# Performance work log

Measured on AMD Instinct MI355X. Metric: run time of the kernel, lower is better.

## Reference

```python
import jax, jax.numpy as jnp
import numpy as np

DIM = 4096
N_HEADS = 32
HEAD_DIM = 128
FFN = 11008
THETA = 10000.0
EPS = 1e-5
B, S, SP = 8, 1, 2048  # batch, decode seq_len, start_pos (valid cache length)


def rmsnorm(x, w):
    return x * jax.lax.rsqrt(jnp.mean(x * x, axis=-1, keepdims=True) + EPS) * w


def apply_rope(x, cos, sin):
    # x: [B, S, H, D]; interleaved-pair complex rotation as in Meta Llama
    xr = x[..., 0::2]
    xi = x[..., 1::2]
    out_r = xr * cos - xi * sin
    out_i = xr * sin + xi * cos
    return jnp.stack([out_r, out_i], axis=-1).reshape(x.shape)


def setup_inputs() -> dict:
    key = jax.random.key(0)
    ks = jax.random.split(key, 10)
    s = 0.02  # weight init scale
    return {
        "x": jax.random.normal(ks[0], (B, S, DIM), jnp.float32),
        "cache_k": jax.random.normal(ks[1], (B, SP, N_HEADS, HEAD_DIM), jnp.float32),
        "cache_v": jax.random.normal(ks[2], (B, SP, N_HEADS, HEAD_DIM), jnp.float32),
        "mask": jnp.zeros((B, N_HEADS, S, SP + S), jnp.float32),
        "wq": jax.random.normal(ks[3], (DIM, DIM), jnp.float32) * s,
        "wk": jax.random.normal(ks[4], (DIM, DIM), jnp.float32) * s,
        "wv": jax.random.normal(ks[5], (DIM, DIM), jnp.float32) * s,
        "wo": jax.random.normal(ks[6], (DIM, DIM), jnp.float32) * s,
        "w1": jax.random.normal(ks[7], (DIM, FFN), jnp.float32) * s,
        "w2": jax.random.normal(ks[8], (FFN, DIM), jnp.float32) * s,
        "w3": jax.random.normal(ks[9], (DIM, FFN), jnp.float32) * s,
        "attn_norm_w": jnp.ones((DIM,), jnp.float32),
        "ffn_norm_w": jnp.ones((DIM,), jnp.float32),
        "start_pos": SP,
    }


def reference(x, cache_k, cache_v, mask, wq, wk, wv, wo, w1, w2, w3, attn_norm_w, ffn_norm_w, start_pos):
    b, s, _ = x.shape
    # --- attention block ---
    h = rmsnorm(x, attn_norm_w)
    q = (h @ wq).reshape(b, s, N_HEADS, HEAD_DIM)
    k = (h @ wk).reshape(b, s, N_HEADS, HEAD_DIM)
    v = (h @ wv).reshape(b, s, N_HEADS, HEAD_DIM)
    # RoPE freqs for positions [start_pos, start_pos+s)
    inv_freq = 1.0 / (THETA ** (jnp.arange(0, HEAD_DIM, 2, dtype=jnp.float32) / HEAD_DIM))
    pos = (start_pos + jnp.arange(s)).astype(jnp.float32)
    ang = pos[:, None] * inv_freq[None, :]            # [s, HEAD_DIM//2]
    cos = jnp.cos(ang)[None, :, None, :]
    sin = jnp.sin(ang)[None, :, None, :]
    q = apply_rope(q, cos, sin)
    k = apply_rope(k, cos, sin)
    # KV cache: valid up to start_pos, append current token
    keys = jnp.concatenate([cache_k, k], axis=1)      # [b, SP+s, H, D]
    vals = jnp.concatenate([cache_v, v], axis=1)
    scores = jnp.einsum("bqhd,bkhd->bhqk", q, keys) / np.sqrt(HEAD_DIM).astype(np.float32)
    scores = scores + mask
    probs = jax.nn.softmax(scores, axis=-1)
    attn = jnp.einsum("bhqk,bkhd->bqhd", probs, vals).reshape(b, s, DIM)
    x = x + attn @ wo
    # --- SwiGLU MLP block ---
    h = rmsnorm(x, ffn_norm_w)
    x = x + (jax.nn.silu(h @ w1) * (h @ w3)) @ w2
    return x
```

## Files before the change

kernel.cpp:

```cpp
#include <hip/hip_runtime.h>
#include <hip/hip_bf16.h>

#define DIMQ 4096
#define NH 32
#define HD 128
#define FFN_D 11008
#define BATCH 8
#define SPQ 2048
#define SEQ 2049
#define NCH 8
#define LN_THETA 9.210340371976184f

__global__ __launch_bounds__(256) void rmsnorm_k(const float* __restrict__ x,
                                                 const float* __restrict__ w,
                                                 float* __restrict__ out) {
    int b = blockIdx.x, tid = threadIdx.x;
    const float* xr = x + b * DIMQ;
    float4 v[4];
    float ss = 0.f;
#pragma unroll
    for (int it = 0; it < 4; ++it) {
        v[it] = *(const float4*)(xr + (it * 256 + tid) * 4);
        ss += v[it].x * v[it].x + v[it].y * v[it].y + v[it].z * v[it].z + v[it].w * v[it].w;
    }
    __shared__ float red[256];
    red[tid] = ss; __syncthreads();
    for (int s = 128; s; s >>= 1) { if (tid < s) red[tid] += red[tid + s]; __syncthreads(); }
    float scale = rsqrtf(red[0] * (1.0f / DIMQ) + 1e-5f);
    float* orow = out + b * DIMQ;
#pragma unroll
    for (int it = 0; it < 4; ++it) {
        float4 wv = *(const float4*)(w + (it * 256 + tid) * 4);
        float4 o;
        o.x = v[it].x * scale * wv.x;
        o.y = v[it].y * scale * wv.y;
        o.z = v[it].z * scale * wv.z;
        o.w = v[it].w * scale * wv.w;
        *(float4*)(orow + (it * 256 + tid) * 4) = o;
    }
}

__global__ __launch_bounds__(256) void gemv_part_k(const float* __restrict__ W0,
                                                   const float* __restrict__ W1m,
                                                   const float* __restrict__ W2m,
                                                   int OUT, int IN,
                                                   const float* __restrict__ act,
                                                   float* __restrict__ P) {
    int tid = threadIdx.x;
    int CH = IN / gridDim.y;
    int i0 = blockIdx.y * CH;
    int TOTC = gridDim.x * 512;
    int effc = blockIdx.x * 512 + tid * 2;
    const float* Wm; int j;
    if (effc < OUT)          { Wm = W0;  j = effc; }
    else if (effc < 2 * OUT) { Wm = W1m; j = effc - OUT; }
    else                     { Wm = W2m; j = effc - 2 * OUT; }
    extern __shared__ float sact[];
    int tot = CH * 8;
    for (int m = tid; m < tot; m += 256)
        sact[m] = act[(m & 7) * IN + i0 + (m >> 3)];
    __syncthreads();
    float2 acc[8];
#pragma unroll
    for (int bb = 0; bb < 8; ++bb) acc[bb] = make_float2(0.f, 0.f);
    const float* wp = Wm + (size_t)i0 * OUT + j;
#pragma unroll 4
    for (int i = 0; i < CH; ++i) {
        float2 wv = *(const float2*)wp; wp += OUT;
        float4 a0 = *(const float4*)(sact + i * 8);
        float4 a1 = *(const float4*)(sact + i * 8 + 4);
        acc[0].x = fmaf(a0.x, wv.x, acc[0].x); acc[0].y = fmaf(a0.x, wv.y, acc[0].y);
        acc[1].x = fmaf(a0.y, wv.x, acc[1].x); acc[1].y = fmaf(a0.y, wv.y, acc[1].y);
        acc[2].x = fmaf(a0.z, wv.x, acc[2].x); acc[2].y = fmaf(a0.z, wv.y, acc[2].y);
        acc[3].x = fmaf(a0.w, wv.x, acc[3].x); acc[3].y = fmaf(a0.w, wv.y, acc[3].y);
        acc[4].x = fmaf(a1.x, wv.x, acc[4].x); acc[4].y = fmaf(a1.x, wv.y, acc[4].y);
        acc[5].x = fmaf(a1.y, wv.x, acc[5].x); acc[5].y = fmaf(a1.y, wv.y, acc[5].y);
        acc[6].x = fmaf(a1.z, wv.x, acc[6].x); acc[6].y = fmaf(a1.z, wv.y, acc[6].y);
        acc[7].x = fmaf(a1.w, wv.x, acc[7].x); acc[7].y = fmaf(a1.w, wv.y, acc[7].y);
    }
    float* pp = P + ((size_t)blockIdx.y * TOTC + effc) * 8;
    *(float4*)(pp)      = make_float4(acc[0].x, acc[1].x, acc[2].x, acc[3].x);
    *(float4*)(pp + 4)  = make_float4(acc[4].x, acc[5].x, acc[6].x, acc[7].x);
    *(float4*)(pp + 8)  = make_float4(acc[0].y, acc[1].y, acc[2].y, acc[3].y);
    *(float4*)(pp + 12) = make_float4(acc[4].y, acc[5].y, acc[6].y, acc[7].y);
}

__global__ __launch_bounds__(256) void reduce_qkv_rope_k(const float* __restrict__ P,
                                                         float* __restrict__ qo,
                                                         float* __restrict__ ko,
                                                         float* __restrict__ vo,
                                                         const int* __restrict__ start_pos,
                                                         int chunks) {
    int tid = threadIdx.x;
    int t = blockIdx.x * 128 + (tid & 127);
    int half = tid >> 7;
    int c0 = half * (chunks >> 1);
    int c1 = half ? chunks : (chunks >> 1);
    float s0 = 0.f, s1 = 0.f, s2 = 0.f, s3 = 0.f;
    int ch = c0;
    for (; ch + 4 <= c1; ch += 4) {
        s0 += P[(size_t)(ch + 0) * 98304 + t];
        s1 += P[(size_t)(ch + 1) * 98304 + t];
        s2 += P[(size_t)(ch + 2) * 98304 + t];
        s3 += P[(size_t)(ch + 3) * 98304 + t];
    }
    for (; ch < c1; ++ch) s0 += P[(size_t)ch * 98304 + t];
    float s = s0 + s1 + s2 + s3;
    __shared__ float red[256];
    red[tid] = s; __syncthreads();
    if (tid < 128) {
        s = red[tid] + red[tid + 128];
        float partner = __shfl_xor(s, 8);
        int b = t & 7, ce = t >> 3;
        int mat = ce >> 12, j = ce & 4095;
        if (mat == 2) {
            vo[b * DIMQ + j] = s;
        } else {
            int d = j & (HD - 1), p = d >> 1;
            float freq = __expf(-(float)(2 * p) * (LN_THETA / (float)HD));
            float ang = (float)start_pos[0] * freq;
            float cs = __cosf(ang), sn = __sinf(ang);
            float val = fmaf(s, cs, (j & 1) ? partner * sn : -partner * sn);
            ((mat == 0) ? qo : ko)[b * DIMQ + j] = val;
        }
    }
}

__global__ __launch_bounds__(256) void attn_part_k(const float* __restrict__ q,
                                                   const float* __restrict__ kn,
                                                   const float* __restrict__ vn,
                                                   const float* __restrict__ ck,
                                                   const float* __restrict__ cv,
                                                   const float* __restrict__ mask,
                                                   float* __restrict__ am,
                                                   float* __restrict__ al,
                                                   float* __restrict__ ao) {
    int c  = blockIdx.x & (NCH - 1);
    int bh = blockIdx.x >> 3;
    int b = bh >> 5, h = bh & 31;
    int tid = threadIdx.x;
    int t0 = c * 256;
    int t1 = (c == NCH - 1) ? SEQ : t0 + 256;
    __shared__ float sc[257];
    __shared__ float red[256];
    __shared__ float2 pvs[4][64];

    int g = tid >> 4, l = tid & 15;
    float qv[8];
    const float* qp = q + b * DIMQ + h * HD + l * 8;
#pragma unroll
    for (int i2 = 0; i2 < 8; ++i2) qv[i2] = qp[i2];
    const float kscale = 0.08838834764831845f;
    const float* mrow = mask + (size_t)(b * NH + h) * SEQ;
    for (int t = t0 + g; t < t1; t += 16) {
        const float* kp = (t < SPQ) ? (ck + ((size_t)(b * SPQ + t) * NH + h) * HD + l * 8)
                                    : (kn + b * DIMQ + h * HD + l * 8);
        float4 k0 = *(const float4*)kp;
        float4 k1 = *(const float4*)(kp + 4);
        float d = qv[0] * k0.x + qv[1] * k0.y + qv[2] * k0.z + qv[3] * k0.w
                + qv[4] * k1.x + qv[5] * k1.y + qv[6] * k1.z + qv[7] * k1.w;
        d += __shfl_xor(d, 1); d += __shfl_xor(d, 2);
        d += __shfl_xor(d, 4); d += __shfl_xor(d, 8);
        if (l == 0) sc[t - t0] = fmaf(d, kscale, mrow[t]);
    }
    __syncthreads();

    int nt = t1 - t0;
    float lm = -1e30f;
    for (int t = tid; t < nt; t += 256) lm = fmaxf(lm, sc[t]);
    red[tid] = lm; __syncthreads();
    for (int s2 = 128; s2; s2 >>= 1) { if (tid < s2) red[tid] = fmaxf(red[tid], red[tid + s2]); __syncthreads(); }
    float m = red[0];
    __syncthreads();
    float ls = 0.f;
    for (int t = tid; t < nt; t += 256) { float p = __expf(sc[t] - m); sc[t] = p; ls += p; }
    red[tid] = ls; __syncthreads();
    for (int s2 = 128; s2; s2 >>= 1) { if (tid < s2) red[tid] += red[tid + s2]; __syncthreads(); }
    float lsum = red[0];

    int dp = tid & 63, q4 = tid >> 6;
    float2 acc = make_float2(0.f, 0.f);
    for (int t = t0 + q4; t < t1; t += 4) {
        float p = sc[t - t0];
        const float* vp = (t < SPQ) ? (cv + ((size_t)(b * SPQ + t) * NH + h) * HD + dp * 2)
                                    : (vn + b * DIMQ + h * HD + dp * 2);
        float2 v2 = *(const float2*)vp;
        acc.x = fmaf(p, v2.x, acc.x);
        acc.y = fmaf(p, v2.y, acc.y);
    }
    pvs[q4][dp] = acc;
    __syncthreads();
    if (tid < 64) {
        float ox = pvs[0][tid].x + pvs[1][tid].x + pvs[2][tid].x + pvs[3][tid].x;
        float oy = pvs[0][tid].y + pvs[1][tid].y + pvs[2][tid].y + pvs[3][tid].y;
        float* op = ao + ((size_t)bh * NCH + c) * HD;
        op[tid * 2]     = ox;
        op[tid * 2 + 1] = oy;
    }
    if (tid == 0) { am[bh * NCH + c] = m; al[bh * NCH + c] = lsum; }
}

__global__ __launch_bounds__(128) void attn_reduce_k(const float* __restrict__ am,
                                                     const float* __restrict__ al,
                                                     const float* __restrict__ ao,
                                                     float* __restrict__ out) {
    int bh = blockIdx.x;
    int b = bh >> 5, h = bh & 31;
    int d = threadIdx.x;
    float mv[NCH];
    float M = -1e30f;
#pragma unroll
    for (int i = 0; i < NCH; ++i) { mv[i] = am[bh * NCH + i]; M = fmaxf(M, mv[i]); }
    float L = 0.f, acc = 0.f;
#pragma unroll
    for (int i = 0; i < NCH; ++i) {
        float w = __expf(mv[i] - M);
        L += al[bh * NCH + i] * w;
        acc += w * ao[((size_t)bh * NCH + i) * HD + d];
    }
    out[b * DIMQ + h * HD + d] = acc / L;
}

__global__ __launch_bounds__(256) void reduce_add_k(const float* __restrict__ P,
                                                    const float* __restrict__ resid,
                                                    float* __restrict__ out,
                                                    int chunks, int n) {
    int tid = threadIdx.x;
    int e = blockIdx.x * 64 + (tid & 63);
    int qr = tid >> 6;
    int c0 = (chunks * qr) >> 2;
    int c1 = (chunks * (qr + 1)) >> 2;
    float s0 = 0.f, s1 = 0.f, s2 = 0.f, s3 = 0.f;
    int ch = c0;
    for (; ch + 4 <= c1; ch += 4) {
        s0 += P[(size_t)(ch + 0) * n + e];
        s1 += P[(size_t)(ch + 1) * n + e];
        s2 += P[(size_t)(ch + 2) * n + e];
        s3 += P[(size_t)(ch + 3) * n + e];
    }
    for (; ch < c1; ++ch) s0 += P[(size_t)ch * n + e];
    __shared__ float red[256];
    red[tid] = s0 + s1 + s2 + s3; __syncthreads();
    if (tid < 64) {
        float s = red[tid] + red[tid + 64] + red[tid + 128] + red[tid + 192];
        int b = e & 7, c = e >> 3;
        out[b * DIMQ + c] = resid[b * DIMQ + c] + s;
    }
}

__global__ __launch_bounds__(256) void reduce_silu_k(const float* __restrict__ P,
                                                     float* __restrict__ e,
                                                     int chunks) {
    int tid = threadIdx.x;
    int t = blockIdx.x * 128 + (tid & 127);
    int half = tid >> 7;
    int c0 = half * (chunks >> 1);
    int c1 = half ? chunks : (chunks >> 1);
    float g0 = 0.f, g1 = 0.f, u0 = 0.f, u1 = 0.f;
    int ch = c0;
    for (; ch + 2 <= c1; ch += 2) {
        g0 += P[(size_t)(ch + 0) * 176128 + t];
        g1 += P[(size_t)(ch + 1) * 176128 + t];
        u0 += P[(size_t)(ch + 0) * 176128 + 88064 + t];
        u1 += P[(size_t)(ch + 1) * 176128 + 88064 + t];
    }
    for (; ch < c1; ++ch) {
        g0 += P[(size_t)ch * 176128 + t];
        u0 += P[(size_t)ch * 176128 + 88064 + t];
    }
    __shared__ float rg[256], ru[256];
    rg[tid] = g0 + g1; ru[tid] = u0 + u1; __syncthreads();
    if (tid < 128) {
        float g = rg[tid] + rg[tid + 128];
        float u = ru[tid] + ru[tid + 128];
        int b = t & 7, c = t >> 3;
        float sg = g / (1.f + __expf(-g));
        e[b * FFN_D + c] = sg * u;
    }
}

extern "C" void kernel_launch(void* const* d_in, const int* in_sizes, int n_in,
                              void* d_out, int out_size, void* d_ws, size_t ws_size,
                              hipStream_t stream) {
    const float* x      = (const float*)d_in[0];
    const float* ck     = (const float*)d_in[1];
    const float* cv     = (const float*)d_in[2];
    const float* mask   = (const float*)d_in[3];
    const float* wq     = (const float*)d_in[4];
    const float* wk     = (const float*)d_in[5];
    const float* wv     = (const float*)d_in[6];
    const float* wo     = (const float*)d_in[7];
    const float* w1     = (const float*)d_in[8];
    const float* w2     = (const float*)d_in[9];
    const float* w3     = (const float*)d_in[10];
    const float* anw    = (const float*)d_in[11];
    const float* fnw    = (const float*)d_in[12];
    const int*   spos   = (const int*)d_in[13];
    float* out = (float*)d_out;

    float* ws = (float*)d_ws;
    float* h    = ws;
    float* qb   = ws + 32768;
    float* kb   = ws + 65536;
    float* vb   = ws + 98304;
    float* attn = ws + 131072;
    float* x1   = ws + 163840;
    float* h2   = ws + 196608;
    float* e    = ws + 229376;
    float* P    = ws + 317440;

    float* am = P;
    float* al = P + 2048;
    float* ao = P + 4096;

    rmsnorm_k<<<BATCH, 256, 0, stream>>>(x, anw, h);
    gemv_part_k<<<dim3(24, 32), 256, 128 * 8 * 4, stream>>>(wq, wk, wv, DIMQ, DIMQ, h, P);
    reduce_qkv_rope_k<<<768, 256, 0, stream>>>(P, qb, kb, vb, spos, 32);
    attn_part_k<<<BATCH * NH * NCH, 256, 0, stream>>>(qb, kb, vb, ck, cv, mask, am, al, ao);
    attn_reduce_k<<<BATCH * NH, 128, 0, stream>>>(am, al, ao, attn);
    gemv_part_k<<<dim3(8, 64), 256, 64 * 8 * 4, stream>>>(wo, wo, wo, DIMQ, DIMQ, attn, P);
    reduce_add_k<<<512, 256, 0, stream>>>(P, x, x1, 64, 32768);
    rmsnorm_k<<<BATCH, 256, 0, stream>>>(x1, fnw, h2);
    gemv_part_k<<<dim3(43, 16), 256, 256 * 8 * 4, stream>>>(w1, w3, w3, FFN_D, DIMQ, h2, P);
    reduce_silu_k<<<688, 256, 0, stream>>>(P, e, 16);
    gemv_part_k<<<dim3(8, 86), 256, 128 * 8 * 4, stream>>>(w2, w2, w2, DIMQ, FFN_D, e, P);
    reduce_add_k<<<512, 256, 0, stream>>>(P, x1, out, 86, 32768);
}
```

Before: 290.1 us.

## Fuse QKV reduction+RoPE into attention and attention merge into Wo GEMV

Removes the separate reduce_qkv_rope and attn_reduce kernels. Each attention block now sums the split-K QKV partials for its own head's q, applies RoPE in shared memory, and only the last chunk block also reduces the new k/v. The Wo GEMV merges the flash-decoding partial softmax results while staging its activations. This saves two launches and the q/k/v/attn round trips through global memory. In exchange, the q reduction is repeated by 8 chunk blocks per head, and the cross-chunk softmax merge is recomputed by every column block of the Wo GEMV.

```diff
diff --git a/kernel.cpp b/kernel.cpp
--- a/kernel.cpp
+++ b/kernel.cpp
@@ -85,53 +85,68 @@
     *(float4*)(pp + 12) = make_float4(acc[4].y, acc[5].y, acc[6].y, acc[7].y);
 }
 
-__global__ __launch_bounds__(256) void reduce_qkv_rope_k(const float* __restrict__ P,
-                                                         float* __restrict__ qo,
-                                                         float* __restrict__ ko,
-                                                         float* __restrict__ vo,
-                                                         const int* __restrict__ start_pos,
-                                                         int chunks) {
-    int tid = threadIdx.x;
-    int t = blockIdx.x * 128 + (tid & 127);
-    int half = tid >> 7;
-    int c0 = half * (chunks >> 1);
-    int c1 = half ? chunks : (chunks >> 1);
-    float s0 = 0.f, s1 = 0.f, s2 = 0.f, s3 = 0.f;
-    int ch = c0;
-    for (; ch + 4 <= c1; ch += 4) {
-        s0 += P[(size_t)(ch + 0) * 98304 + t];
-        s1 += P[(size_t)(ch + 1) * 98304 + t];
-        s2 += P[(size_t)(ch + 2) * 98304 + t];
-        s3 += P[(size_t)(ch + 3) * 98304 + t];
-    }
-    for (; ch < c1; ++ch) s0 += P[(size_t)ch * 98304 + t];
-    float s = s0 + s1 + s2 + s3;
-    __shared__ float red[256];
-    red[tid] = s; __syncthreads();
-    if (tid < 128) {
-        s = red[tid] + red[tid + 128];
-        float partner = __shfl_xor(s, 8);
-        int b = t & 7, ce = t >> 3;
-        int mat = ce >> 12, j = ce & 4095;
-        if (mat == 2) {
-            vo[b * DIMQ + j] = s;
-        } else {
-            int d = j & (HD - 1), p = d >> 1;
-            float freq = __expf(-(float)(2 * p) * (LN_THETA / (float)HD));
-            float ang = (float)start_pos[0] * freq;
-            float cs = __cosf(ang), sn = __sinf(ang);
-            float val = fmaf(s, cs, (j & 1) ? partner * sn : -partner * sn);
-            ((mat == 0) ? qo : ko)[b * DIMQ + j] = val;
-        }
-    }
-}
-
-__global__ __launch_bounds__(256) void attn_part_k(const float* __restrict__ q,
-                                                   const float* __restrict__ kn,
-                                                   const float* __restrict__ vn,
+__global__ __launch_bounds__(256) void gemv_wo_k(const float* __restrict__ W,
+                                                 const float* __restrict__ am,
+                                                 const float* __restrict__ al,
+                                                 const float* __restrict__ ao,
+                                                 float* __restrict__ P) {
+    int tid = threadIdx.x;
+    int CH = DIMQ / gridDim.y;
+    int i0 = blockIdx.y * CH;
+    int TOTC = gridDim.x * 512;
+    int effc = blockIdx.x * 512 + tid * 2;
+    const float* Wm = W; int j = effc;
+    extern __shared__ float sact[];
+    int tot = CH * 8;
+    for (int m = tid; m < tot; m += 256) {
+        int b = m & 7, row = m >> 3;
+        int j2 = i0 + row;
+        int hh = j2 >> 7, dd = j2 & 127;
+        int bh = b * NH + hh;
+        float mv[NCH];
+        float M = -1e30f;
+#pragma unroll
+        for (int i = 0; i < NCH; ++i) { mv[i] = am[bh * NCH + i]; M = fmaxf(M, mv[i]); }
+        float L = 0.f, acc = 0.f;
+#pragma unroll
+        for (int i = 0; i < NCH; ++i) {
+            float w = __expf(mv[i] - M);
+            L += al[bh * NCH + i] * w;
+            acc += w * ao[((size_t)bh * NCH + i) * HD + dd];
+        }
+        sact[m] = acc / L;
+    }
+    __syncthreads();
+    float2 acc[8];
+#pragma unroll
+    for (int bb = 0; bb < 8; ++bb) acc[bb] = make_float2(0.f, 0.f);
+    const float* wp = Wm + (size_t)i0 * DIMQ + j;
+#pragma unroll 4
+    for (int i = 0; i < CH; ++i) {
+        float2 wv = *(const float2*)wp; wp += DIMQ;
+        float4 a0 = *(const float4*)(sact + i * 8);
+        float4 a1 = *(const float4*)(sact + i * 8 + 4);
+        acc[0].x = fmaf(a0.x, wv.x, acc[0].x); acc[0].y = fmaf(a0.x, wv.y, acc[0].y);
+        acc[1].x = fmaf(a0.y, wv.x, acc[1].x); acc[1].y = fmaf(a0.y, wv.y, acc[1].y);
+        acc[2].x = fmaf(a0.z, wv.x, acc[2].x); acc[2].y = fmaf(a0.z, wv.y, acc[2].y);
+        acc[3].x = fmaf(a0.w, wv.x, acc[3].x); acc[3].y = fmaf(a0.w, wv.y, acc[3].y);
+        acc[4].x = fmaf(a1.x, wv.x, acc[4].x); acc[4].y = fmaf(a1.x, wv.y, acc[4].y);
+        acc[5].x = fmaf(a1.y, wv.x, acc[5].x); acc[5].y = fmaf(a1.y, wv.y, acc[5].y);
+        acc[6].x = fmaf(a1.z, wv.x, acc[6].x); acc[6].y = fmaf(a1.z, wv.y, acc[6].y);
+        acc[7].x = fmaf(a1.w, wv.x, acc[7].x); acc[7].y = fmaf(a1.w, wv.y, acc[7].y);
+    }
+    float* pp = P + ((size_t)blockIdx.y * TOTC + effc) * 8;
+    *(float4*)(pp)      = make_float4(acc[0].x, acc[1].x, acc[2].x, acc[3].x);
+    *(float4*)(pp + 4)  = make_float4(acc[4].x, acc[5].x, acc[6].x, acc[7].x);
+    *(float4*)(pp + 8)  = make_float4(acc[0].y, acc[1].y, acc[2].y, acc[3].y);
+    *(float4*)(pp + 12) = make_float4(acc[4].y, acc[5].y, acc[6].y, acc[7].y);
+}
+
+__global__ __launch_bounds__(256) void attn_part_k(const float* __restrict__ P,
                                                    const float* __restrict__ ck,
                                                    const float* __restrict__ cv,
                                                    const float* __restrict__ mask,
+                                                   const int* __restrict__ start_pos,
                                                    float* __restrict__ am,
                                                    float* __restrict__ al,
                                                    float* __restrict__ ao) {
@@ -141,27 +156,86 @@
     int tid = threadIdx.x;
     int t0 = c * 256;
     int t1 = (c == NCH - 1) ? SEQ : t0 + 256;
+    __shared__ float sq[HD];
+    __shared__ float skn[HD], svn[HD];
     __shared__ float sc[257];
     __shared__ float red[256];
     __shared__ float2 pvs[4][64];
 
+    int d = tid & 127, sh = tid >> 7;
+    float spos_f = (float)start_pos[0];
+    {
+        float s = 0.f;
+        int tq = (h * HD + d) * 8 + b;
+        for (int ch = sh * 16; ch < sh * 16 + 16; ++ch)
+            s += P[(size_t)ch * 98304 + tq];
+        red[tid] = s;
+    }
+    __syncthreads();
+    if (tid < 128) sc[d] = red[tid] + red[tid + 128];
+    __syncthreads();
+    if (tid < 128) {
+        int p = d >> 1;
+        float freq = __expf(-(float)(2 * p) * (LN_THETA / (float)HD));
+        float ang = spos_f * freq;
+        float cs = __cosf(ang), sn = __sinf(ang);
+        float partner = sc[d ^ 1];
+        sq[d] = fmaf(sc[d], cs, (d & 1) ? partner * sn : -partner * sn);
+    }
+    __syncthreads();
+    if (c == NCH - 1) {
+        {
+            float s = 0.f;
+            int tk = (DIMQ + h * HD + d) * 8 + b;
+            for (int ch = sh * 16; ch < sh * 16 + 16; ++ch)
+                s += P[(size_t)ch * 98304 + tk];
+            red[tid] = s;
+        }
+        __syncthreads();
+        if (tid < 128) sc[d] = red[tid] + red[tid + 128];
+        __syncthreads();
+        if (tid < 128) {
+            int p = d >> 1;
+            float freq = __expf(-(float)(2 * p) * (LN_THETA / (float)HD));
+            float ang = spos_f * freq;
+            float cs = __cosf(ang), sn = __sinf(ang);
+            float partner = sc[d ^ 1];
+            skn[d] = fmaf(sc[d], cs, (d & 1) ? partner * sn : -partner * sn);
+        }
+        __syncthreads();
+        {
+            float s = 0.f;
+            int tv = (2 * DIMQ + h * HD + d) * 8 + b;
+            for (int ch = sh * 16; ch < sh * 16 + 16; ++ch)
+                s += P[(size_t)ch * 98304 + tv];
+            red[tid] = s;
+        }
+        __syncthreads();
+        if (tid < 128) svn[d] = red[tid] + red[tid + 128];
+        __syncthreads();
+    }
+
     int g = tid >> 4, l = tid & 15;
     float qv[8];
-    const float* qp = q + b * DIMQ + h * HD + l * 8;
-#pragma unroll
-    for (int i2 = 0; i2 < 8; ++i2) qv[i2] = qp[i2];
+#pragma unroll
+    for (int i2 = 0; i2 < 8; ++i2) qv[i2] = sq[l * 8 + i2];
     const float kscale = 0.08838834764831845f;
     const float* mrow = mask + (size_t)(b * NH + h) * SEQ;
     for (int t = t0 + g; t < t1; t += 16) {
-        const float* kp = (t < SPQ) ? (ck + ((size_t)(b * SPQ + t) * NH + h) * HD + l * 8)
-                                    : (kn + b * DIMQ + h * HD + l * 8);
-        float4 k0 = *(const float4*)kp;
-        float4 k1 = *(const float4*)(kp + 4);
-        float d = qv[0] * k0.x + qv[1] * k0.y + qv[2] * k0.z + qv[3] * k0.w
-                + qv[4] * k1.x + qv[5] * k1.y + qv[6] * k1.z + qv[7] * k1.w;
-        d += __shfl_xor(d, 1); d += __shfl_xor(d, 2);
-        d += __shfl_xor(d, 4); d += __shfl_xor(d, 8);
-        if (l == 0) sc[t - t0] = fmaf(d, kscale, mrow[t]);
+        float4 k0, k1;
+        if (t < SPQ) {
+            const float* kp = ck + ((size_t)(b * SPQ + t) * NH + h) * HD + l * 8;
+            k0 = *(const float4*)kp;
+            k1 = *(const float4*)(kp + 4);
+        } else {
+            k0 = *(const float4*)(skn + l * 8);
+            k1 = *(const float4*)(skn + l * 8 + 4);
+        }
+        float dd = qv[0] * k0.x + qv[1] * k0.y + qv[2] * k0.z + qv[3] * k0.w
+                 + qv[4] * k1.x + qv[5] * k1.y + qv[6] * k1.z + qv[7] * k1.w;
+        dd += __shfl_xor(dd, 1); dd += __shfl_xor(dd, 2);
+        dd += __shfl_xor(dd, 4); dd += __shfl_xor(dd, 8);
+        if (l == 0) sc[t - t0] = fmaf(dd, kscale, mrow[t]);
     }
     __syncthreads();
 
@@ -182,9 +256,12 @@
     float2 acc = make_float2(0.f, 0.f);
     for (int t = t0 + q4; t < t1; t += 4) {
         float p = sc[t - t0];
-        const float* vp = (t < SPQ) ? (cv + ((size_t)(b * SPQ + t) * NH + h) * HD + dp * 2)
-                                    : (vn + b * DIMQ + h * HD + dp * 2);
-        float2 v2 = *(const float2*)vp;
+        float2 v2;
+        if (t < SPQ) {
+            v2 = *(const float2*)(cv + ((size_t)(b * SPQ + t) * NH + h) * HD + dp * 2);
+        } else {
+            v2 = *(const float2*)(svn + dp * 2);
+        }
         acc.x = fmaf(p, v2.x, acc.x);
         acc.y = fmaf(p, v2.y, acc.y);
     }
@@ -198,27 +275,6 @@
         op[tid * 2 + 1] = oy;
     }
     if (tid == 0) { am[bh * NCH + c] = m; al[bh * NCH + c] = lsum; }
-}
-
-__global__ __launch_bounds__(128) void attn_reduce_k(const float* __restrict__ am,
-                                                     const float* __restrict__ al,
-                                                     const float* __restrict__ ao,
-                                                     float* __restrict__ out) {
-    int bh = blockIdx.x;
-    int b = bh >> 5, h = bh & 31;
-    int d = threadIdx.x;
-    float mv[NCH];
-    float M = -1e30f;
-#pragma unroll
-    for (int i = 0; i < NCH; ++i) { mv[i] = am[bh * NCH + i]; M = fmaxf(M, mv[i]); }
-    float L = 0.f, acc = 0.f;
-#pragma unroll
-    for (int i = 0; i < NCH; ++i) {
-        float w = __expf(mv[i] - M);
-        L += al[bh * NCH + i] * w;
-        acc += w * ao[((size_t)bh * NCH + i) * HD + d];
-    }
-    out[b * DIMQ + h * HD + d] = acc / L;
 }
 
 __global__ __launch_bounds__(256) void reduce_add_k(const float* __restrict__ P,
@@ -300,25 +356,19 @@
 
     float* ws = (float*)d_ws;
     float* h    = ws;
-    float* qb   = ws + 32768;
-    float* kb   = ws + 65536;
-    float* vb   = ws + 98304;
-    float* attn = ws + 131072;
     float* x1   = ws + 163840;
     float* h2   = ws + 196608;
     float* e    = ws + 229376;
     float* P    = ws + 317440;
 
-    float* am = P;
-    float* al = P + 2048;
-    float* ao = P + 4096;
+    float* am = P + 3145728;
+    float* al = am + 2048;
+    float* ao = al + 2048;
 
     rmsnorm_k<<<BATCH, 256, 0, stream>>>(x, anw, h);
     gemv_part_k<<<dim3(24, 32), 256, 128 * 8 * 4, stream>>>(wq, wk, wv, DIMQ, DIMQ, h, P);
-    reduce_qkv_rope_k<<<768, 256, 0, stream>>>(P, qb, kb, vb, spos, 32);
-    attn_part_k<<<BATCH * NH * NCH, 256, 0, stream>>>(qb, kb, vb, ck, cv, mask, am, al, ao);
-    attn_reduce_k<<<BATCH * NH, 128, 0, stream>>>(am, al, ao, attn);
-    gemv_part_k<<<dim3(8, 64), 256, 64 * 8 * 4, stream>>>(wo, wo, wo, DIMQ, DIMQ, attn, P);
+    attn_part_k<<<BATCH * NH * NCH, 256, 0, stream>>>(P, ck, cv, mask, spos, am, al, ao);
+    gemv_wo_k<<<dim3(8, 64), 256, 64 * 8 * 4, stream>>>(wo, am, al, ao, P);
     reduce_add_k<<<512, 256, 0, stream>>>(P, x, x1, 64, 32768);
     rmsnorm_k<<<BATCH, 256, 0, stream>>>(x1, fnw, h2);
     gemv_part_k<<<dim3(43, 16), 256, 256 * 8 * 4, stream>>>(w1, w3, w3, FFN_D, DIMQ, h2, P);
```

Measured after the change: 351.7 us. 1.21x slower.

## Store GEMV activations feature-major so staging uses contiguous float4 loads

Applied to the files above, without the earlier changes.

The producers of GEMV activations (rmsnorm, attention reduce, silu reduce) now write their outputs transposed as [feature][batch]. The GEMV kernel can then stage its activation chunk into shared memory with contiguous float4 copies instead of strided gathers across batch rows. The cost moves to the producers, which now do strided scalar stores. Those tensors are small, so the gain is limited to the staging phase of each GEMV.

```diff
diff --git a/kernel.cpp b/kernel.cpp
--- a/kernel.cpp
+++ b/kernel.cpp
@@ -27,16 +27,14 @@
     red[tid] = ss; __syncthreads();
     for (int s = 128; s; s >>= 1) { if (tid < s) red[tid] += red[tid + s]; __syncthreads(); }
     float scale = rsqrtf(red[0] * (1.0f / DIMQ) + 1e-5f);
-    float* orow = out + b * DIMQ;
 #pragma unroll
     for (int it = 0; it < 4; ++it) {
-        float4 wv = *(const float4*)(w + (it * 256 + tid) * 4);
-        float4 o;
-        o.x = v[it].x * scale * wv.x;
-        o.y = v[it].y * scale * wv.y;
-        o.z = v[it].z * scale * wv.z;
-        o.w = v[it].w * scale * wv.w;
-        *(float4*)(orow + (it * 256 + tid) * 4) = o;
+        int j = (it * 256 + tid) * 4;
+        float4 wv = *(const float4*)(w + j);
+        out[(j + 0) * 8 + b] = v[it].x * scale * wv.x;
+        out[(j + 1) * 8 + b] = v[it].y * scale * wv.y;
+        out[(j + 2) * 8 + b] = v[it].z * scale * wv.z;
+        out[(j + 3) * 8 + b] = v[it].w * scale * wv.w;
     }
 }
 
@@ -44,7 +42,7 @@
                                                    const float* __restrict__ W1m,
                                                    const float* __restrict__ W2m,
                                                    int OUT, int IN,
-                                                   const float* __restrict__ act,
+                                                   const float* __restrict__ actT,
                                                    float* __restrict__ P) {
     int tid = threadIdx.x;
     int CH = IN / gridDim.y;
@@ -56,9 +54,10 @@
     else if (effc < 2 * OUT) { Wm = W1m; j = effc - OUT; }
     else                     { Wm = W2m; j = effc - 2 * OUT; }
     extern __shared__ float sact[];
-    int tot = CH * 8;
-    for (int m = tid; m < tot; m += 256)
-        sact[m] = act[(m & 7) * IN + i0 + (m >> 3)];
+    int tot4 = (CH * 8) >> 2;
+    const float4* src = (const float4*)(actT + (size_t)i0 * 8);
+    for (int m = tid; m < tot4; m += 256)
+        ((float4*)sact)[m] = src[m];
     __syncthreads();
     float2 acc[8];
 #pragma unroll
@@ -203,7 +202,7 @@
 __global__ __launch_bounds__(128) void attn_reduce_k(const float* __restrict__ am,
                                                      const float* __restrict__ al,
                                                      const float* __restrict__ ao,
-                                                     float* __restrict__ out) {
+                                                     float* __restrict__ outT) {
     int bh = blockIdx.x;
     int b = bh >> 5, h = bh & 31;
     int d = threadIdx.x;
@@ -218,7 +217,7 @@
         L += al[bh * NCH + i] * w;
         acc += w * ao[((size_t)bh * NCH + i) * HD + d];
     }
-    out[b * DIMQ + h * HD + d] = acc / L;
+    outT[(h * HD + d) * 8 + b] = acc / L;
 }
 
 __global__ __launch_bounds__(256) void reduce_add_k(const float* __restrict__ P,
@@ -249,7 +248,7 @@
 }
 
 __global__ __launch_bounds__(256) void reduce_silu_k(const float* __restrict__ P,
-                                                     float* __restrict__ e,
+                                                     float* __restrict__ eT,
                                                      int chunks) {
     int tid = threadIdx.x;
     int t = blockIdx.x * 128 + (tid & 127);
@@ -273,9 +272,8 @@
     if (tid < 128) {
         float g = rg[tid] + rg[tid + 128];
         float u = ru[tid] + ru[tid + 128];
-        int b = t & 7, c = t >> 3;
         float sg = g / (1.f + __expf(-g));
-        e[b * FFN_D + c] = sg * u;
+        eT[t] = sg * u;
     }
 }
 
@@ -299,30 +297,30 @@
     float* out = (float*)d_out;
 
     float* ws = (float*)d_ws;
-    float* h    = ws;
+    float* hT   = ws;
     float* qb   = ws + 32768;
     float* kb   = ws + 65536;
     float* vb   = ws + 98304;
-    float* attn = ws + 131072;
+    float* attnT= ws + 131072;
     float* x1   = ws + 163840;
-    float* h2   = ws + 196608;
-    float* e    = ws + 229376;
+    float* h2T  = ws + 196608;
+    float* eT   = ws + 229376;
     float* P    = ws + 317440;
 
     float* am = P;
     float* al = P + 2048;
     float* ao = P + 4096;
 
-    rmsnorm_k<<<BATCH, 256, 0, stream>>>(x, anw, h);
-    gemv_part_k<<<dim3(24, 32), 256, 128 * 8 * 4, stream>>>(wq, wk, wv, DIMQ, DIMQ, h, P);
+    rmsnorm_k<<<BATCH, 256, 0, stream>>>(x, anw, hT);
+    gemv_part_k<<<dim3(24, 32), 256, 128 * 8 * 4, stream>>>(wq, wk, wv, DIMQ, DIMQ, hT, P);
     reduce_qkv_rope_k<<<768, 256, 0, stream>>>(P, qb, kb, vb, spos, 32);
     attn_part_k<<<BATCH * NH * NCH, 256, 0, stream>>>(qb, kb, vb, ck, cv, mask, am, al, ao);
-    attn_reduce_k<<<BATCH * NH, 128, 0, stream>>>(am, al, ao, attn);
-    gemv_part_k<<<dim3(8, 64), 256, 64 * 8 * 4, stream>>>(wo, wo, wo, DIMQ, DIMQ, attn, P);
+    attn_reduce_k<<<BATCH * NH, 128, 0, stream>>>(am, al, ao, attnT);
+    gemv_part_k<<<dim3(8, 64), 256, 64 * 8 * 4, stream>>>(wo, wo, wo, DIMQ, DIMQ, attnT, P);
     reduce_add_k<<<512, 256, 0, stream>>>(P, x, x1, 64, 32768);
-    rmsnorm_k<<<BATCH, 256, 0, stream>>>(x1, fnw, h2);
-    gemv_part_k<<<dim3(43, 16), 256, 256 * 8 * 4, stream>>>(w1, w3, w3, FFN_D, DIMQ, h2, P);
-    reduce_silu_k<<<688, 256, 0, stream>>>(P, e, 16);
-    gemv_part_k<<<dim3(8, 86), 256, 128 * 8 * 4, stream>>>(w2, w2, w2, DIMQ, FFN_D, e, P);
+    rmsnorm_k<<<BATCH, 256, 0, stream>>>(x1, fnw, h2T);
+    gemv_part_k<<<dim3(43, 16), 256, 256 * 8 * 4, stream>>>(w1, w3, w3, FFN_D, DIMQ, h2T, P);
+    reduce_silu_k<<<688, 256, 0, stream>>>(P, eT, 16);
+    gemv_part_k<<<dim3(8, 86), 256, 128 * 8 * 4, stream>>>(w2, w2, w2, DIMQ, FFN_D, eT, P);
     reduce_add_k<<<512, 256, 0, stream>>>(P, x1, out, 86, 32768);
 }
```

Result: no change. 289.0 us, median of 2 (-0.4%).
